# Optimization experiments

Measured on AMD Instinct MI355X. Metric: run time of the kernel, lower is better.

Reference implementation:

```python
import jax, jax.numpy as jnp
import numpy as np

K = 7  # kernel_size from init


def setup_inputs() -> dict:
    key = jax.random.key(0)
    ks = jax.random.split(key, 4)
    B, C, H, W = 8, 64, 384, 384
    x = jax.random.normal(ks[0], (B, C, H, W), dtype=jnp.float32)
    w1 = jax.random.normal(ks[1], (16, C), dtype=jnp.float32) * (1.0 / np.sqrt(C))
    b1 = jnp.zeros((16,), dtype=jnp.float32)
    w2 = jax.random.normal(ks[2], (3, 16), dtype=jnp.float32) * 0.25
    b2 = jnp.zeros((3,), dtype=jnp.float32)
    return {"x": x, "w1": w1, "b1": b1, "w2": w2, "b2": b2}


def reference(x, w1, b1, w2, b2):
    B, C, H, W = x.shape
    # param predictor: global avg pool -> 1x1 conv (dense) -> SiLU -> 1x1 conv (dense)
    pooled = x.mean(axis=(2, 3))                       # [B, C]
    h = jax.nn.silu(pooled @ w1.T + b1)                # [B, 16]
    p = h @ w2.T + b2                                  # [B, 3]
    sigma = jax.nn.softplus(p[:, 0])                   # [B]
    dx = jnp.tanh(p[:, 1]) * 2.0
    dy = jnp.tanh(p[:, 2]) * 2.0
    # per-sample Gaussian kernels, vectorized over batch
    coords = jnp.arange(K, dtype=x.dtype)
    gy, gx = jnp.meshgrid(coords, coords, indexing="ij")  # [K, K]
    cx = (K - 1) / 2.0 + dx                            # [B]
    cy = (K - 1) / 2.0 + dy
    g = jnp.exp(-((gx[None] - cx[:, None, None]) ** 2 + (gy[None] - cy[:, None, None]) ** 2)
                / (2.0 * sigma[:, None, None] ** 2))   # [B, K, K]
    g = g / g.sum(axis=(1, 2), keepdims=True)
    # depthwise conv with per-sample kernel via groups = B*C
    kernels = jnp.broadcast_to(g[:, None], (B, C, K, K)).reshape(B * C, 1, K, K)
    out = jax.lax.conv_general_dilated(
        x.reshape(1, B * C, H, W), kernels,
        window_strides=(1, 1), padding=[(K // 2, K // 2)] * 2,
        feature_group_count=B * C,
        dimension_numbers=("NCHW", "OIHW", "NCHW"))
    return out.reshape(B, C, H, W)
```

## Files before the change

### kernel.cpp

```cpp
#include <hip/hip_runtime.h>
#include <math.h>

#define IMG_W 384
#define IMG_H 384
#define IMG_HW (IMG_W * IMG_H)
#define N_IMG 512
#define N_CH 64
#define N_B 8

__global__ __launch_bounds__(256) void pool_kernel(const float* __restrict__ x,
                                                   float* __restrict__ pooled) {
    const int bc = blockIdx.x;
    const float4* xp = (const float4*)(x + (size_t)bc * IMG_HW);
    const int t = threadIdx.x;
    float s = 0.f;
    #pragma unroll 4
    for (int k = 0; k < 144; ++k) {
        float4 v = xp[t + k * 256];
        s += (v.x + v.y) + (v.z + v.w);
    }
    #pragma unroll
    for (int off = 32; off > 0; off >>= 1) s += __shfl_down(s, off, 64);
    __shared__ float red[4];
    if ((t & 63) == 0) red[t >> 6] = s;
    __syncthreads();
    if (t == 0) {
        float tot = (red[0] + red[1]) + (red[2] + red[3]);
        pooled[bc] = tot * (1.0f / (float)IMG_HW);
    }
}

__global__ void params_kernel(const float* __restrict__ pooled,
                              const float* __restrict__ w1, const float* __restrict__ b1,
                              const float* __restrict__ w2, const float* __restrict__ b2,
                              float* __restrict__ guv) {
    const int b = threadIdx.x;
    if (b >= N_B) return;
    const float* P = pooled + b * N_CH;
    float h[16];
    #pragma unroll
    for (int j = 0; j < 16; ++j) {
        float acc = b1[j];
        for (int c = 0; c < N_CH; ++c) acc += P[c] * w1[j * N_CH + c];
        h[j] = acc / (1.f + expf(-acc));
    }
    float p[3];
    #pragma unroll
    for (int k = 0; k < 3; ++k) {
        float acc = b2[k];
        #pragma unroll
        for (int j = 0; j < 16; ++j) acc += h[j] * w2[k * 16 + j];
        p[k] = acc;
    }
    float sigma = (p[0] > 20.f) ? p[0] : log1pf(expf(p[0]));
    float dx = tanhf(p[1]) * 2.f;
    float dy = tanhf(p[2]) * 2.f;
    float cx = 3.f + dx, cy = 3.f + dy;
    float inv2s2 = 1.f / (2.f * sigma * sigma);
    float u[7], v[7], su = 0.f, sv = 0.f;
    #pragma unroll
    for (int i = 0; i < 7; ++i) { float d = (float)i - cx; u[i] = expf(-d * d * inv2s2); su += u[i]; }
    #pragma unroll
    for (int j = 0; j < 7; ++j) { float d = (float)j - cy; v[j] = expf(-d * d * inv2s2); sv += v[j]; }
    float rsu = 1.f / su, rsv = 1.f / sv;
    #pragma unroll
    for (int i = 0; i < 7; ++i) guv[b * 14 + i] = u[i] * rsu;
    #pragma unroll
    for (int j = 0; j < 7; ++j) guv[b * 14 + 7 + j] = v[j] * rsv;
}

__global__ __launch_bounds__(384) void conv_kernel(const float* __restrict__ x,
                                                   const float* __restrict__ guv,
                                                   float* __restrict__ out) {
    __shared__ float buf[2][8][392];
    const int tid = threadIdx.x;
    const int bc = blockIdx.x;
    const int b = bc >> 6;
    const float* img = x + (size_t)bc * IMG_HW;
    float* oimg = out + (size_t)bc * IMG_HW;

    float u[7], v[7];
    #pragma unroll
    for (int i = 0; i < 7; ++i) { u[i] = guv[b * 14 + i]; v[i] = guv[b * 14 + 7 + i]; }

    if (tid < 128) {
        int r = tid >> 3;
        int p = tid & 7;
        int col = (p < 4) ? p : (384 + p);
        buf[r >> 3][r & 7][col] = 0.f;
    }

    for (int q = tid; q < 576; q += 384) {
        int brow = q / 96;
        int c4 = (q % 96) * 4;
        int row = -3 + brow;
        float4 val = make_float4(0.f, 0.f, 0.f, 0.f);
        if (row >= 0) val = *(const float4*)(img + row * IMG_W + c4);
        *(float4*)&buf[1][brow][4 + c4] = val;
    }
    #pragma unroll
    for (int k = 0; k < 2; ++k) {
        int q = tid + k * 384;
        int brow = q / 96;
        int c4 = (q % 96) * 4;
        float4 val = *(const float4*)(img + (3 + brow) * IMG_W + c4);
        *(float4*)&buf[0][brow][4 + c4] = val;
    }
    __syncthreads();

    const int xc = tid + 1;
    float h[6];
    #pragma unroll
    for (int k = 0; k < 6; ++k) {
        float a = 0.f;
        #pragma unroll
        for (int i = 0; i < 7; ++i) a += u[i] * buf[1][k][xc + i];
        h[k] = a;
    }

    for (int c = 0; c < 48; ++c) {
        __syncthreads();
        float4 nv[2];
        int brow_[2], c4_[2];
        const bool have_next = (c + 1 < 48);
        if (have_next) {
            int r0 = 8 * (c + 1) + 3;
            #pragma unroll
            for (int k = 0; k < 2; ++k) {
                int q = tid + k * 384;
                brow_[k] = q / 96;
                c4_[k] = (q % 96) * 4;
                int row = r0 + brow_[k];
                nv[k] = make_float4(0.f, 0.f, 0.f, 0.f);
                if (row < IMG_H) nv[k] = *(const float4*)(img + row * IMG_W + c4_[k]);
            }
        }
        const float (*bufc)[392] = buf[c & 1];
        const int ybase = 8 * c;
        #pragma unroll
        for (int r = 0; r < 8; ++r) {
            float hn = 0.f;
            #pragma unroll
            for (int i = 0; i < 7; ++i) hn += u[i] * bufc[r][xc + i];
            float o = v[0] * h[0] + v[1] * h[1] + v[2] * h[2] + v[3] * h[3]
                    + v[4] * h[4] + v[5] * h[5] + v[6] * hn;
            oimg[(ybase + r) * IMG_W + tid] = o;
            #pragma unroll
            for (int k = 0; k < 5; ++k) h[k] = h[k + 1];
            h[5] = hn;
        }
        if (have_next) {
            float (*bufn)[392] = buf[(c + 1) & 1];
            #pragma unroll
            for (int k = 0; k < 2; ++k) {
                *(float4*)&bufn[brow_[k]][4 + c4_[k]] = nv[k];
            }
        }
    }
}

extern "C" void kernel_launch(void* const* d_in, const int* in_sizes, int n_in,
                              void* d_out, int out_size, void* d_ws, size_t ws_size,
                              hipStream_t stream) {
    const float* x  = (const float*)d_in[0];
    const float* w1 = (const float*)d_in[1];
    const float* b1 = (const float*)d_in[2];
    const float* w2 = (const float*)d_in[3];
    const float* b2 = (const float*)d_in[4];
    float* outp = (float*)d_out;

    float* pooled = (float*)d_ws;
    float* guv    = pooled + 512;

    pool_kernel<<<N_IMG, 256, 0, stream>>>(x, pooled);
    params_kernel<<<1, 64, 0, stream>>>(pooled, w1, b1, w2, b2, guv);
    conv_kernel<<<N_IMG, 384, 0, stream>>>(x, guv, outp);
}
```

Before: 598.5 us.

## Split pool and conv into more blocks with float4 row-band conv tiling

```diff
diff --git a/kernel.cpp b/kernel.cpp
--- a/kernel.cpp
+++ b/kernel.cpp
@@ -7,36 +7,46 @@
 #define N_IMG 512
 #define N_CH 64
 #define N_B 8
+#define POOL_PARTS 4
 
 __global__ __launch_bounds__(256) void pool_kernel(const float* __restrict__ x,
-                                                   float* __restrict__ pooled) {
-    const int bc = blockIdx.x;
-    const float4* xp = (const float4*)(x + (size_t)bc * IMG_HW);
+                                                   float* __restrict__ partial) {
+    const int blk = blockIdx.x;
+    const int bc = blk >> 2;
+    const int part = blk & 3;
+    const float4* xp = (const float4*)(x + (size_t)bc * IMG_HW + part * (IMG_HW / POOL_PARTS));
     const int t = threadIdx.x;
-    float s = 0.f;
-    #pragma unroll 4
-    for (int k = 0; k < 144; ++k) {
-        float4 v = xp[t + k * 256];
-        s += (v.x + v.y) + (v.z + v.w);
+    float s0 = 0.f, s1 = 0.f;
+    #pragma unroll
+    for (int k = 0; k < 36; k += 2) {
+        float4 a = xp[t + k * 256];
+        float4 b = xp[t + (k + 1) * 256];
+        s0 += (a.x + a.y) + (a.z + a.w);
+        s1 += (b.x + b.y) + (b.z + b.w);
     }
+    float s = s0 + s1;
     #pragma unroll
     for (int off = 32; off > 0; off >>= 1) s += __shfl_down(s, off, 64);
     __shared__ float red[4];
     if ((t & 63) == 0) red[t >> 6] = s;
     __syncthreads();
-    if (t == 0) {
-        float tot = (red[0] + red[1]) + (red[2] + red[3]);
-        pooled[bc] = tot * (1.0f / (float)IMG_HW);
-    }
+    if (t == 0) partial[blk] = (red[0] + red[1]) + (red[2] + red[3]);
 }
 
-__global__ void params_kernel(const float* __restrict__ pooled,
+__global__ __launch_bounds__(512) void params_kernel(const float* __restrict__ partial,
                               const float* __restrict__ w1, const float* __restrict__ b1,
                               const float* __restrict__ w2, const float* __restrict__ b2,
                               float* __restrict__ guv) {
-    const int b = threadIdx.x;
+    __shared__ float pooled[N_IMG];
+    const int t = threadIdx.x;
+    {
+        float4 pp = *(const float4*)(partial + t * 4);
+        pooled[t] = (pp.x + pp.y + pp.z + pp.w) * (1.0f / (float)IMG_HW);
+    }
+    __syncthreads();
+    const int b = t;
     if (b >= N_B) return;
-    const float* P = pooled + b * N_CH;
+    const float* P = &pooled[b * N_CH];
     float h[16];
     #pragma unroll
     for (int j = 0; j < 16; ++j) {
@@ -69,15 +79,27 @@
     for (int j = 0; j < 7; ++j) guv[b * 14 + 7 + j] = v[j] * rsv;
 }
 
+#define BANDS 2
+#define BAND_ROWS 192
+#define GROUP_ROWS 48
+#define NITER 27
+#define LROW 392
+
 __global__ __launch_bounds__(384) void conv_kernel(const float* __restrict__ x,
                                                    const float* __restrict__ guv,
                                                    float* __restrict__ out) {
-    __shared__ float buf[2][8][392];
+    __shared__ float buf[2][8][LROW];
     const int tid = threadIdx.x;
-    const int bc = blockIdx.x;
+    const int tx = tid % 96;
+    const int ty = tid / 96;
+    const int blk = blockIdx.x;
+    const int bc = blk >> 1;
+    const int band = blk & 1;
     const int b = bc >> 6;
     const float* img = x + (size_t)bc * IMG_HW;
     float* oimg = out + (size_t)bc * IMG_HW;
+    const int base4 = 4 * tx;
+    const int gbase = band * BAND_ROWS + ty * GROUP_ROWS;
 
     float u[7], v[7];
     #pragma unroll
@@ -90,72 +112,70 @@
         buf[r >> 3][r & 7][col] = 0.f;
     }
 
-    for (int q = tid; q < 576; q += 384) {
-        int brow = q / 96;
-        int c4 = (q % 96) * 4;
-        int row = -3 + brow;
-        float4 val = make_float4(0.f, 0.f, 0.f, 0.f);
-        if (row >= 0) val = *(const float4*)(img + row * IMG_W + c4);
-        *(float4*)&buf[1][brow][4 + c4] = val;
-    }
     #pragma unroll
     for (int k = 0; k < 2; ++k) {
-        int q = tid + k * 384;
-        int brow = q / 96;
-        int c4 = (q % 96) * 4;
-        float4 val = *(const float4*)(img + (3 + brow) * IMG_W + c4);
-        *(float4*)&buf[0][brow][4 + c4] = val;
+        int s = ty + 4 * k;
+        int g = s >> 1, sub = s & 1;
+        int row = band * BAND_ROWS + g * GROUP_ROWS - 3 + sub;
+        float4 val = make_float4(0.f, 0.f, 0.f, 0.f);
+        if (row >= 0 && row < IMG_H) val = *(const float4*)(img + row * IMG_W + base4);
+        *(float4*)&buf[0][s][4 + base4] = val;
     }
     __syncthreads();
 
-    const int xc = tid + 1;
-    float h[6];
+    float4 h[6];
     #pragma unroll
-    for (int k = 0; k < 6; ++k) {
-        float a = 0.f;
-        #pragma unroll
-        for (int i = 0; i < 7; ++i) a += u[i] * buf[1][k][xc + i];
-        h[k] = a;
-    }
+    for (int k = 0; k < 6; ++k) h[k] = make_float4(0.f, 0.f, 0.f, 0.f);
 
-    for (int c = 0; c < 48; ++c) {
-        __syncthreads();
+    for (int it = 0; it < NITER; ++it) {
         float4 nv[2];
-        int brow_[2], c4_[2];
-        const bool have_next = (c + 1 < 48);
+        const bool have_next = (it + 1 < NITER);
         if (have_next) {
-            int r0 = 8 * (c + 1) + 3;
             #pragma unroll
             for (int k = 0; k < 2; ++k) {
-                int q = tid + k * 384;
-                brow_[k] = q / 96;
-                c4_[k] = (q % 96) * 4;
-                int row = r0 + brow_[k];
+                int s = ty + 4 * k;
+                int g = s >> 1, sub = s & 1;
+                int row = band * BAND_ROWS + g * GROUP_ROWS + 2 * (it + 1) - 3 + sub;
                 nv[k] = make_float4(0.f, 0.f, 0.f, 0.f);
-                if (row < IMG_H) nv[k] = *(const float4*)(img + row * IMG_W + c4_[k]);
+                if (row >= 0 && row < IMG_H) nv[k] = *(const float4*)(img + row * IMG_W + base4);
             }
         }
-        const float (*bufc)[392] = buf[c & 1];
-        const int ybase = 8 * c;
+        const float (*cb)[LROW] = buf[it & 1];
         #pragma unroll
-        for (int r = 0; r < 8; ++r) {
-            float hn = 0.f;
+        for (int r = 0; r < 2; ++r) {
+            const float* rp = &cb[ty * 2 + r][base4];
+            float4 a  = *(const float4*)(rp);
+            float4 bq = *(const float4*)(rp + 4);
+            float4 cq = *(const float4*)(rp + 8);
+            float wv[12] = {a.x, a.y, a.z, a.w, bq.x, bq.y, bq.z, bq.w,
+                            cq.x, cq.y, cq.z, cq.w};
+            float4 hn;
+            hn.x = u[0]*wv[1] + u[1]*wv[2] + u[2]*wv[3] + u[3]*wv[4] + u[4]*wv[5] + u[5]*wv[6] + u[6]*wv[7];
+            hn.y = u[0]*wv[2] + u[1]*wv[3] + u[2]*wv[4] + u[3]*wv[5] + u[4]*wv[6] + u[5]*wv[7] + u[6]*wv[8];
+            hn.z = u[0]*wv[3] + u[1]*wv[4] + u[2]*wv[5] + u[3]*wv[6] + u[4]*wv[7] + u[5]*wv[8] + u[6]*wv[9];
+            hn.w = u[0]*wv[4] + u[1]*wv[5] + u[2]*wv[6] + u[3]*wv[7] + u[4]*wv[8] + u[5]*wv[9] + u[6]*wv[10];
+            if (it >= 3) {
+                const int y = gbase + 2 * (it - 3) + r;
+                float4 o;
+                o.x = v[0]*h[0].x + v[1]*h[1].x + v[2]*h[2].x + v[3]*h[3].x + v[4]*h[4].x + v[5]*h[5].x + v[6]*hn.x;
+                o.y = v[0]*h[0].y + v[1]*h[1].y + v[2]*h[2].y + v[3]*h[3].y + v[4]*h[4].y + v[5]*h[5].y + v[6]*hn.y;
+                o.z = v[0]*h[0].z + v[1]*h[1].z + v[2]*h[2].z + v[3]*h[3].z + v[4]*h[4].z + v[5]*h[5].z + v[6]*hn.z;
+                o.w = v[0]*h[0].w + v[1]*h[1].w + v[2]*h[2].w + v[3]*h[3].w + v[4]*h[4].w + v[5]*h[5].w + v[6]*hn.w;
+                *(float4*)(oimg + y * IMG_W + base4) = o;
+            }
             #pragma unroll
-            for (int i = 0; i < 7; ++i) hn += u[i] * bufc[r][xc + i];
-            float o = v[0] * h[0] + v[1] * h[1] + v[2] * h[2] + v[3] * h[3]
-                    + v[4] * h[4] + v[5] * h[5] + v[6] * hn;
-            oimg[(ybase + r) * IMG_W + tid] = o;
-            #pragma unroll
-            for (int k = 0; k < 5; ++k) h[k] = h[k + 1];
+            for (int k2 = 0; k2 < 5; ++k2) h[k2] = h[k2 + 1];
             h[5] = hn;
         }
         if (have_next) {
-            float (*bufn)[392] = buf[(c + 1) & 1];
+            float (*bn)[LROW] = buf[(it + 1) & 1];
             #pragma unroll
             for (int k = 0; k < 2; ++k) {
-                *(float4*)&bufn[brow_[k]][4 + c4_[k]] = nv[k];
+                int s = ty + 4 * k;
+                *(float4*)&bn[s][4 + base4] = nv[k];
             }
         }
+        __syncthreads();
     }
 }
 
@@ -169,10 +189,10 @@
     const float* b2 = (const float*)d_in[4];
     float* outp = (float*)d_out;
 
-    float* pooled = (float*)d_ws;
-    float* guv    = pooled + 512;
+    float* partial = (float*)d_ws;
+    float* guv     = partial + 2048;
 
-    pool_kernel<<<N_IMG, 256, 0, stream>>>(x, pooled);
-    params_kernel<<<1, 64, 0, stream>>>(pooled, w1, b1, w2, b2, guv);
-    conv_kernel<<<N_IMG, 384, 0, stream>>>(x, guv, outp);
+    pool_kernel<<<N_IMG * POOL_PARTS, 256, 0, stream>>>(x, partial);
+    params_kernel<<<1, 512, 0, stream>>>(partial, w1, b1, w2, b2, guv);
+    conv_kernel<<<N_IMG * BANDS, 384, 0, stream>>>(x, guv, outp);
 }
```

After: 588.9 us. Within noise of the previous version (-1.6%).
